# Kernel tuning notes

Hardware: AMD Instinct MI355X
Metric: run time of the kernel (lower is better)

Reference implementation:

```python
import jax, jax.numpy as jnp
import numpy as np

N_NODES = 100000
N_EDGES = 1600000
D_FEAT = 128
D_EMB = 128
ROUNDS = 4
M_OUT = 32
NUM_GRAPHS = 512


def setup_inputs() -> dict:
    key = jax.random.key(0)
    ks = jax.random.split(key, 12)
    x = jax.random.normal(ks[0], (N_NODES, D_FEAT), dtype=jnp.float32)
    edge_index = jax.random.randint(ks[1], (2, N_EDGES), 0, N_NODES, dtype=jnp.int32)
    batch = jnp.sort(jax.random.randint(ks[2], (N_NODES,), 0, NUM_GRAPHS, dtype=jnp.int32))
    s = 1.0 / np.sqrt(D_EMB)
    emb_W = jax.random.uniform(ks[3], (D_FEAT, D_EMB), minval=-s, maxval=s, dtype=jnp.float32)
    emb_b = jax.random.uniform(ks[4], (D_EMB,), minval=-s, maxval=s, dtype=jnp.float32)
    msg_W = jax.random.uniform(ks[5], (ROUNDS, D_EMB, D_EMB), minval=-s, maxval=s, dtype=jnp.float32)
    msg_b = jax.random.uniform(ks[6], (ROUNDS, D_EMB), minval=-s, maxval=s, dtype=jnp.float32)
    upd_W = jax.random.uniform(ks[7], (ROUNDS, D_EMB, D_EMB), minval=-s, maxval=s, dtype=jnp.float32)
    upd_b = jax.random.uniform(ks[8], (ROUNDS, D_EMB), minval=-s, maxval=s, dtype=jnp.float32)
    out_W = jax.random.uniform(ks[9], (D_EMB, M_OUT), minval=-s, maxval=s, dtype=jnp.float32)
    out_b = jax.random.uniform(ks[10], (M_OUT,), minval=-s, maxval=s, dtype=jnp.float32)
    return {"x": x, "edge_index": edge_index, "batch": batch,
            "emb_W": emb_W, "emb_b": emb_b, "msg_W": msg_W, "msg_b": msg_b,
            "upd_W": upd_W, "upd_b": upd_b, "out_W": out_W, "out_b": out_b}


def reference(x, edge_index, batch, emb_W, emb_b, msg_W, msg_b, upd_W, upd_b, out_W, out_b):
    src, dst = edge_index[0], edge_index[1]
    # initial node embedding: Linear + ReLU
    state = jax.nn.relu(x @ emb_W + emb_b)  # [N, D]
    for r in range(ROUNDS):
        message = jax.nn.relu(state @ msg_W[r] + msg_b[r])      # [N, D]
        # gather messages along edges, scatter-add to destination nodes
        aggregated = jax.ops.segment_sum(message[src], dst, num_segments=N_NODES)  # [N, D]
        state = state + jax.nn.relu(aggregated @ upd_W[r] + upd_b[r])
    # sum-pool nodes into graphs
    graph_state = jax.ops.segment_sum(state, batch, num_segments=NUM_GRAPHS)  # [G, D]
    return graph_state @ out_W + out_b  # [G, M]
```

## Files before the change

kernel.cpp:

```cpp
#include <hip/hip_runtime.h>

#define N_NODES    100000
#define N_EDGES    1600000
#define D_EMB      128
#define ROUNDS     4
#define M_OUT      32
#define NUM_GRAPHS 512

#define SCAN_ELEMS_PER_BLOCK 1024
#define SCAN_NBLK ((N_NODES + SCAN_ELEMS_PER_BLOCK - 1) / SCAN_ELEMS_PER_BLOCK)

typedef __attribute__((ext_vector_type(8))) short short8;
typedef __attribute__((ext_vector_type(4))) float f32x4;

static __device__ __forceinline__ unsigned short f2bf(float f) {
    union { float f; unsigned u; } v; v.f = f;
    unsigned u = v.u;
    unsigned r = (u + 0x7FFFu + ((u >> 16) & 1u)) >> 16;
    return (unsigned short)r;
}
static __device__ __forceinline__ float bf2f(unsigned short h) {
    union { unsigned u; float f; } v; v.u = ((unsigned)h) << 16;
    return v.f;
}

__global__ __launch_bounds__(256) void prep_weights_kernel(
    const float* __restrict__ emb_W, const float* __restrict__ msg_W,
    const float* __restrict__ upd_W, unsigned short* __restrict__ WTall)
{
    const int mi = blockIdx.x;
    const float* W = (mi == 0) ? emb_W
                   : (mi <= 4) ? msg_W + (size_t)(mi - 1) * D_EMB * D_EMB
                               : upd_W + (size_t)(mi - 5) * D_EMB * D_EMB;
    unsigned short* WT = WTall + (size_t)mi * D_EMB * D_EMB;
    for (int idx = threadIdx.x; idx < D_EMB * D_EMB; idx += 256) {
        const int n = idx >> 7, k = idx & 127;
        WT[idx] = f2bf(W[k * D_EMB + n]);
    }
}

template<int MODE, bool AF32>
__global__ __launch_bounds__(256) void gemm_mfma_kernel(
    const void* __restrict__ Aptr, const unsigned short* __restrict__ WT,
    const float* __restrict__ bias, float* __restrict__ state_f32,
    unsigned short* __restrict__ out_bf16)
{
    __shared__ unsigned short As[32][136];

    const int tid = threadIdx.x;
    const int r0  = blockIdx.x * 32;

    if (AF32) {
        const float4* A4 = (const float4*)Aptr + (size_t)r0 * 32;
        #pragma unroll
        for (int i = 0; i < 4; ++i) {
            const int ch = tid + (i << 8);
            const int r = ch >> 5, c = (ch & 31) << 2;
            const float4 f = A4[ch];
            ushort4 h;
            h.x = f2bf(f.x); h.y = f2bf(f.y); h.z = f2bf(f.z); h.w = f2bf(f.w);
            *(ushort4*)&As[r][c] = h;
        }
    } else {
        const uint4* A4 = (const uint4*)((const unsigned short*)Aptr + (size_t)r0 * D_EMB);
        #pragma unroll
        for (int i = 0; i < 2; ++i) {
            const int ch = tid + (i << 8);
            const int r = ch >> 4, c = (ch & 15) << 3;
            *(uint4*)&As[r][c] = A4[ch];
        }
    }
    __syncthreads();

    const int lane = tid & 63;
    const int w    = tid >> 6;
    const int m    = lane & 15;
    const int g    = lane >> 4;

    short8 a[2][4];
    #pragma unroll
    for (int rt = 0; rt < 2; ++rt)
        #pragma unroll
        for (int ks = 0; ks < 4; ++ks)
            a[rt][ks] = *(const short8*)&As[rt * 16 + m][ks * 32 + g * 8];

    short8 b[2][4];
    #pragma unroll
    for (int ct = 0; ct < 2; ++ct) {
        const int n = w * 32 + ct * 16 + m;
        #pragma unroll
        for (int ks = 0; ks < 4; ++ks)
            b[ct][ks] = *(const short8*)&WT[n * D_EMB + ks * 32 + g * 8];
    }

    f32x4 acc[2][2] = {};
    #pragma unroll
    for (int ks = 0; ks < 4; ++ks)
        #pragma unroll
        for (int rt = 0; rt < 2; ++rt)
            #pragma unroll
            for (int ct = 0; ct < 2; ++ct)
                acc[rt][ct] = __builtin_amdgcn_mfma_f32_16x16x32_bf16(
                    a[rt][ks], b[ct][ks], acc[rt][ct], 0, 0, 0);

    #pragma unroll
    for (int rt = 0; rt < 2; ++rt) {
        #pragma unroll
        for (int ct = 0; ct < 2; ++ct) {
            const int col = w * 32 + ct * 16 + m;
            const float bv = bias[col];
            #pragma unroll
            for (int r = 0; r < 4; ++r) {
                const int row = r0 + rt * 16 + g * 4 + r;
                const float v = fmaxf(acc[rt][ct][r] + bv, 0.f);
                const size_t idx = (size_t)row * D_EMB + col;
                if (MODE == 0) {
                    out_bf16[idx] = f2bf(v);
                } else if (MODE == 2) {
                    state_f32[idx] = v;
                    out_bf16[idx] = f2bf(v);
                } else {
                    const float s = state_f32[idx] + v;
                    state_f32[idx] = s;
                    out_bf16[idx] = f2bf(s);
                }
            }
        }
    }
}

__global__ __launch_bounds__(256) void hist_kernel(
    const int* __restrict__ dst, int* __restrict__ deg)
{
    const int e = blockIdx.x * 256 + threadIdx.x;
    if (e < N_EDGES) atomicAdd(&deg[dst[e]], 1);
}

__global__ __launch_bounds__(256) void scan_local_kernel(
    const int* __restrict__ deg, int* __restrict__ rp, int* __restrict__ partials)
{
    __shared__ int sm[256];
    const int tid  = threadIdx.x;
    const int base = blockIdx.x * SCAN_ELEMS_PER_BLOCK + tid * 4;

    int v0 = (base + 0 < N_NODES) ? deg[base + 0] : 0;
    int v1 = (base + 1 < N_NODES) ? deg[base + 1] : 0;
    int v2 = (base + 2 < N_NODES) ? deg[base + 2] : 0;
    int v3 = (base + 3 < N_NODES) ? deg[base + 3] : 0;
    const int tot = v0 + v1 + v2 + v3;

    sm[tid] = tot;
    __syncthreads();
    #pragma unroll
    for (int off = 1; off < 256; off <<= 1) {
        const int x = (tid >= off) ? sm[tid - off] : 0;
        __syncthreads();
        sm[tid] += x;
        __syncthreads();
    }
    const int bex = sm[tid] - tot;

    if (base + 0 < N_NODES) rp[base + 0] = bex;
    if (base + 1 < N_NODES) rp[base + 1] = bex + v0;
    if (base + 2 < N_NODES) rp[base + 2] = bex + v0 + v1;
    if (base + 3 < N_NODES) rp[base + 3] = bex + v0 + v1 + v2;
    if (tid == 255) partials[blockIdx.x] = sm[255];
}

__global__ __launch_bounds__(128) void scan_partials_kernel(int* __restrict__ partials)
{
    __shared__ int sm[128];
    const int tid = threadIdx.x;
    const int v = (tid < SCAN_NBLK) ? partials[tid] : 0;
    sm[tid] = v;
    __syncthreads();
    #pragma unroll
    for (int off = 1; off < 128; off <<= 1) {
        const int x = (tid >= off) ? sm[tid - off] : 0;
        __syncthreads();
        sm[tid] += x;
        __syncthreads();
    }
    if (tid < SCAN_NBLK) partials[tid] = sm[tid] - v;
}

__global__ __launch_bounds__(256) void scan_fixup_kernel(
    int* __restrict__ rp, const int* __restrict__ partials, int* __restrict__ pos)
{
    const int i = blockIdx.x * 256 + threadIdx.x;
    if (i < N_NODES) {
        const int v = rp[i] + partials[i >> 10];
        rp[i] = v;
        pos[i] = v;
    }
    if (i == 0) rp[N_NODES] = N_EDGES;
}

__global__ __launch_bounds__(256) void fill_kernel(
    const int* __restrict__ src, const int* __restrict__ dst,
    int* __restrict__ pos, int* __restrict__ esrc)
{
    const int e = blockIdx.x * 256 + threadIdx.x;
    if (e < N_EDGES) {
        const int idx = atomicAdd(&pos[dst[e]], 1);
        esrc[idx] = src[e];
    }
}

__global__ __launch_bounds__(256) void gather_bf16_kernel(
    const unsigned short* __restrict__ msg, const int* __restrict__ rp,
    const int* __restrict__ esrc, unsigned short* __restrict__ agg)
{
    const int tid = threadIdx.x;
    const int j   = tid & 15;
    const int n   = blockIdx.x * 16 + (tid >> 4);
    if (n >= N_NODES) return;

    const int beg = rp[n];
    const int end = rp[n + 1];
    const uint4* m4 = (const uint4*)msg;

    float a0[8] = {0,0,0,0,0,0,0,0};
    float a1[8] = {0,0,0,0,0,0,0,0};
    int i = beg;
    for (; i + 1 < end; i += 2) {
        const int s0 = esrc[i];
        const int s1 = esrc[i + 1];
        const uint4 v0 = m4[(size_t)s0 * 16 + j];
        const uint4 v1 = m4[(size_t)s1 * 16 + j];
        a0[0] += bf2f(v0.x & 0xffff); a0[1] += bf2f(v0.x >> 16);
        a0[2] += bf2f(v0.y & 0xffff); a0[3] += bf2f(v0.y >> 16);
        a0[4] += bf2f(v0.z & 0xffff); a0[5] += bf2f(v0.z >> 16);
        a0[6] += bf2f(v0.w & 0xffff); a0[7] += bf2f(v0.w >> 16);
        a1[0] += bf2f(v1.x & 0xffff); a1[1] += bf2f(v1.x >> 16);
        a1[2] += bf2f(v1.y & 0xffff); a1[3] += bf2f(v1.y >> 16);
        a1[4] += bf2f(v1.z & 0xffff); a1[5] += bf2f(v1.z >> 16);
        a1[6] += bf2f(v1.w & 0xffff); a1[7] += bf2f(v1.w >> 16);
    }
    if (i < end) {
        const uint4 v0 = m4[(size_t)esrc[i] * 16 + j];
        a0[0] += bf2f(v0.x & 0xffff); a0[1] += bf2f(v0.x >> 16);
        a0[2] += bf2f(v0.y & 0xffff); a0[3] += bf2f(v0.y >> 16);
        a0[4] += bf2f(v0.z & 0xffff); a0[5] += bf2f(v0.z >> 16);
        a0[6] += bf2f(v0.w & 0xffff); a0[7] += bf2f(v0.w >> 16);
    }
    #pragma unroll
    for (int t = 0; t < 8; ++t) a0[t] += a1[t];

    uint4 o;
    o.x = (unsigned)f2bf(a0[0]) | ((unsigned)f2bf(a0[1]) << 16);
    o.y = (unsigned)f2bf(a0[2]) | ((unsigned)f2bf(a0[3]) << 16);
    o.z = (unsigned)f2bf(a0[4]) | ((unsigned)f2bf(a0[5]) << 16);
    o.w = (unsigned)f2bf(a0[6]) | ((unsigned)f2bf(a0[7]) << 16);
    ((uint4*)agg)[(size_t)n * 16 + j] = o;
}

__global__ __launch_bounds__(256) void pool_kernel(
    const float* __restrict__ state, const int* __restrict__ batch,
    float* __restrict__ gs)
{
    const int tid = threadIdx.x;
    const int c = tid & 127;
    const int h = tid >> 7;
    const int n0 = blockIdx.x * 64 + h * 32;

    float acc = 0.f;
    int cur = -1;
    for (int i = 0; i < 32; ++i) {
        const int n = n0 + i;
        if (n >= N_NODES) break;
        const int bb = batch[n];
        if (bb != cur) {
            if (cur >= 0) unsafeAtomicAdd(&gs[cur * D_EMB + c], acc);
            cur = bb;
            acc = 0.f;
        }
        acc += state[(size_t)n * D_EMB + c];
    }
    if (cur >= 0) unsafeAtomicAdd(&gs[cur * D_EMB + c], acc);
}

__global__ __launch_bounds__(256) void out_kernel(
    const float* __restrict__ gs, const float* __restrict__ W,
    const float* __restrict__ bias, float* __restrict__ out)
{
    const int idx = blockIdx.x * 256 + threadIdx.x;
    const int g = idx >> 5;
    const int m = idx & 31;
    float acc = 0.f;
    #pragma unroll 8
    for (int k = 0; k < D_EMB; ++k)
        acc += gs[g * D_EMB + k] * W[k * M_OUT + m];
    out[idx] = acc + bias[m];
}

extern "C" void kernel_launch(void* const* d_in, const int* in_sizes, int n_in,
                              void* d_out, int out_size, void* d_ws, size_t ws_size,
                              hipStream_t stream)
{
    const float* x     = (const float*)d_in[0];
    const int*   eidx  = (const int*)d_in[1];
    const int*   batch = (const int*)d_in[2];
    const float* emb_W = (const float*)d_in[3];
    const float* emb_b = (const float*)d_in[4];
    const float* msg_W = (const float*)d_in[5];
    const float* msg_b = (const float*)d_in[6];
    const float* upd_W = (const float*)d_in[7];
    const float* upd_b = (const float*)d_in[8];
    const float* out_W = (const float*)d_in[9];
    const float* out_b = (const float*)d_in[10];
    float* out = (float*)d_out;

    const int* src = eidx;
    const int* dst = eidx + N_EDGES;

    char* p = (char*)d_ws;
    float* state_f32 = (float*)p;                       p += (size_t)N_NODES * D_EMB * 4;
    unsigned short* state_bf16 = (unsigned short*)p;    p += (size_t)N_NODES * D_EMB * 2;
    unsigned short* msg_bf16 = (unsigned short*)p;      p += (size_t)N_NODES * D_EMB * 2;
    unsigned short* agg_bf16 = (unsigned short*)p;      p += (size_t)N_NODES * D_EMB * 2;
    float* gs = (float*)p;                              p += (size_t)NUM_GRAPHS * D_EMB * 4;
    unsigned short* WTall = (unsigned short*)p;         p += (size_t)9 * D_EMB * D_EMB * 2;
    int* rp = (int*)p;                                  p += (size_t)(N_NODES + 1) * 4;
    int* esrc = (int*)p;                                p += (size_t)N_EDGES * 4;
    int* partials = (int*)p;

    int* deg = (int*)msg_bf16;
    int* pos = (int*)agg_bf16;

    const dim3 blk(256);
    const int gemm_grid = N_NODES / 32;

    prep_weights_kernel<<<9, blk, 0, stream>>>(emb_W, msg_W, upd_W, WTall);
    hipMemsetAsync(deg, 0, (size_t)N_NODES * sizeof(int), stream);
    hist_kernel<<<(N_EDGES + 255) / 256, blk, 0, stream>>>(dst, deg);
    scan_local_kernel<<<SCAN_NBLK, blk, 0, stream>>>(deg, rp, partials);
    scan_partials_kernel<<<1, 128, 0, stream>>>(partials);
    scan_fixup_kernel<<<(SCAN_NBLK * SCAN_ELEMS_PER_BLOCK) / 256, blk, 0, stream>>>(rp, partials, pos);
    fill_kernel<<<(N_EDGES + 255) / 256, blk, 0, stream>>>(src, dst, pos, esrc);

    gemm_mfma_kernel<2, true><<<gemm_grid, blk, 0, stream>>>(
        x, WTall, emb_b, state_f32, state_bf16);

    for (int r = 0; r < ROUNDS; ++r) {
        gemm_mfma_kernel<0, false><<<gemm_grid, blk, 0, stream>>>(
            state_bf16, WTall + (size_t)(1 + r) * D_EMB * D_EMB,
            msg_b + (size_t)r * D_EMB, nullptr, msg_bf16);
        gather_bf16_kernel<<<(N_NODES + 15) / 16, blk, 0, stream>>>(
            msg_bf16, rp, esrc, agg_bf16);
        gemm_mfma_kernel<1, false><<<gemm_grid, blk, 0, stream>>>(
            agg_bf16, WTall + (size_t)(5 + r) * D_EMB * D_EMB,
            upd_b + (size_t)r * D_EMB, state_f32, state_bf16);
    }

    hipMemsetAsync(gs, 0, (size_t)NUM_GRAPHS * D_EMB * sizeof(float), stream);
    pool_kernel<<<(N_NODES + 63) / 64, blk, 0, stream>>>(state_f32, batch, gs);
    out_kernel<<<(NUM_GRAPHS * M_OUT) / 256, blk, 0, stream>>>(gs, out_W, out_b, out);
}
```

Measured before the change: 700.8 us.

## Use persistent double-buffered GEMM, bf16-only state, and multipass CSR build

The GEMM becomes a persistent kernel of 1024 blocks. Each block loads its weight fragments once and double-buffers the A tiles through shared memory, prefetching the next tile into registers. The fp32 state copy is dropped and the residual state is kept only in bf16, which cuts write and read traffic in the update GEMM and in pooling, at the cost of extra rounding across rounds. The histogram and CSR fill kernels now make 8 passes, each restricted to one destination range, to localise atomics. The pool kernel reads the bf16 state two channels per thread.

```diff
diff --git a/kernel.cpp b/kernel.cpp
--- a/kernel.cpp
+++ b/kernel.cpp
@@ -6,6 +6,11 @@
 #define ROUNDS     4
 #define M_OUT      32
 #define NUM_GRAPHS 512
+
+#define NPASS      8
+#define PASS_RANGE (N_NODES / NPASS)
+#define GEMM_BLOCKS 1024
+#define N_TILES    (N_NODES / 32)
 
 #define SCAN_ELEMS_PER_BLOCK 1024
 #define SCAN_NBLK ((N_NODES + SCAN_ELEMS_PER_BLOCK - 1) / SCAN_ELEMS_PER_BLOCK)
@@ -40,100 +45,148 @@
 }
 
 template<int MODE, bool AF32>
-__global__ __launch_bounds__(256) void gemm_mfma_kernel(
+__global__ __launch_bounds__(256) void gemm_loop_kernel(
     const void* __restrict__ Aptr, const unsigned short* __restrict__ WT,
-    const float* __restrict__ bias, float* __restrict__ state_f32,
-    unsigned short* __restrict__ out_bf16)
-{
-    __shared__ unsigned short As[32][136];
-
-    const int tid = threadIdx.x;
-    const int r0  = blockIdx.x * 32;
-
-    if (AF32) {
-        const float4* A4 = (const float4*)Aptr + (size_t)r0 * 32;
-        #pragma unroll
-        for (int i = 0; i < 4; ++i) {
-            const int ch = tid + (i << 8);
-            const int r = ch >> 5, c = (ch & 31) << 2;
-            const float4 f = A4[ch];
-            ushort4 h;
-            h.x = f2bf(f.x); h.y = f2bf(f.y); h.z = f2bf(f.z); h.w = f2bf(f.w);
-            *(ushort4*)&As[r][c] = h;
-        }
-    } else {
-        const uint4* A4 = (const uint4*)((const unsigned short*)Aptr + (size_t)r0 * D_EMB);
-        #pragma unroll
-        for (int i = 0; i < 2; ++i) {
-            const int ch = tid + (i << 8);
-            const int r = ch >> 4, c = (ch & 15) << 3;
-            *(uint4*)&As[r][c] = A4[ch];
-        }
-    }
-    __syncthreads();
-
+    const float* __restrict__ bias, unsigned short* __restrict__ state,
+    unsigned short* __restrict__ outb)
+{
+    __shared__ unsigned short As[2][32][136];
+
+    const int tid  = threadIdx.x;
     const int lane = tid & 63;
     const int w    = tid >> 6;
     const int m    = lane & 15;
     const int g    = lane >> 4;
 
-    short8 a[2][4];
-    #pragma unroll
-    for (int rt = 0; rt < 2; ++rt)
-        #pragma unroll
-        for (int ks = 0; ks < 4; ++ks)
-            a[rt][ks] = *(const short8*)&As[rt * 16 + m][ks * 32 + g * 8];
-
-    short8 b[2][4];
+    short8 bfr[2][4];
     #pragma unroll
     for (int ct = 0; ct < 2; ++ct) {
         const int n = w * 32 + ct * 16 + m;
         #pragma unroll
         for (int ks = 0; ks < 4; ++ks)
-            b[ct][ks] = *(const short8*)&WT[n * D_EMB + ks * 32 + g * 8];
-    }
-
-    f32x4 acc[2][2] = {};
-    #pragma unroll
-    for (int ks = 0; ks < 4; ++ks)
+            bfr[ct][ks] = *(const short8*)&WT[n * D_EMB + ks * 32 + g * 8];
+    }
+    const float bv0 = bias[w * 32 + m];
+    const float bv1 = bias[w * 32 + 16 + m];
+
+    int tile = blockIdx.x;
+
+    if (AF32) {
+        const float4* A4 = (const float4*)Aptr;
+        #pragma unroll
+        for (int i = 0; i < 4; ++i) {
+            const int ch = tid + (i << 8);
+            const float4 f = A4[(size_t)tile * 1024 + ch];
+            ushort4 h; h.x = f2bf(f.x); h.y = f2bf(f.y); h.z = f2bf(f.z); h.w = f2bf(f.w);
+            *(ushort4*)&As[0][ch >> 5][(ch & 31) << 2] = h;
+        }
+    } else {
+        const uint4* A2 = (const uint4*)Aptr;
+        #pragma unroll
+        for (int i = 0; i < 2; ++i) {
+            const int ch = tid + (i << 8);
+            const uint4 v = A2[(size_t)tile * 512 + ch];
+            *(uint4*)&As[0][ch >> 4][(ch & 15) << 3] = v;
+        }
+    }
+    __syncthreads();
+
+    int cur = 0;
+    while (true) {
+        const int next = tile + GEMM_BLOCKS;
+        const bool have = next < N_TILES;
+
+        float4 rgf[4]; uint4 rgu[2];
+        if (have) {
+            if (AF32) {
+                const float4* A4 = (const float4*)Aptr;
+                #pragma unroll
+                for (int i = 0; i < 4; ++i)
+                    rgf[i] = A4[(size_t)next * 1024 + tid + (i << 8)];
+            } else {
+                const uint4* A2 = (const uint4*)Aptr;
+                #pragma unroll
+                for (int i = 0; i < 2; ++i)
+                    rgu[i] = A2[(size_t)next * 512 + tid + (i << 8)];
+            }
+        }
+
+        short8 a[2][4];
         #pragma unroll
         for (int rt = 0; rt < 2; ++rt)
             #pragma unroll
-            for (int ct = 0; ct < 2; ++ct)
-                acc[rt][ct] = __builtin_amdgcn_mfma_f32_16x16x32_bf16(
-                    a[rt][ks], b[ct][ks], acc[rt][ct], 0, 0, 0);
-
-    #pragma unroll
-    for (int rt = 0; rt < 2; ++rt) {
-        #pragma unroll
-        for (int ct = 0; ct < 2; ++ct) {
-            const int col = w * 32 + ct * 16 + m;
-            const float bv = bias[col];
+            for (int ks = 0; ks < 4; ++ks)
+                a[rt][ks] = *(const short8*)&As[cur][rt * 16 + m][ks * 32 + g * 8];
+
+        f32x4 acc[2][2] = {};
+        #pragma unroll
+        for (int ks = 0; ks < 4; ++ks)
             #pragma unroll
-            for (int r = 0; r < 4; ++r) {
-                const int row = r0 + rt * 16 + g * 4 + r;
-                const float v = fmaxf(acc[rt][ct][r] + bv, 0.f);
-                const size_t idx = (size_t)row * D_EMB + col;
-                if (MODE == 0) {
-                    out_bf16[idx] = f2bf(v);
-                } else if (MODE == 2) {
-                    state_f32[idx] = v;
-                    out_bf16[idx] = f2bf(v);
-                } else {
-                    const float s = state_f32[idx] + v;
-                    state_f32[idx] = s;
-                    out_bf16[idx] = f2bf(s);
+            for (int rt = 0; rt < 2; ++rt)
+                #pragma unroll
+                for (int ct = 0; ct < 2; ++ct)
+                    acc[rt][ct] = __builtin_amdgcn_mfma_f32_16x16x32_bf16(
+                        a[rt][ks], bfr[ct][ks], acc[rt][ct], 0, 0, 0);
+
+        if (have) {
+            if (AF32) {
+                #pragma unroll
+                for (int i = 0; i < 4; ++i) {
+                    const int ch = tid + (i << 8);
+                    ushort4 h;
+                    h.x = f2bf(rgf[i].x); h.y = f2bf(rgf[i].y);
+                    h.z = f2bf(rgf[i].z); h.w = f2bf(rgf[i].w);
+                    *(ushort4*)&As[cur ^ 1][ch >> 5][(ch & 31) << 2] = h;
+                }
+            } else {
+                #pragma unroll
+                for (int i = 0; i < 2; ++i) {
+                    const int ch = tid + (i << 8);
+                    *(uint4*)&As[cur ^ 1][ch >> 4][(ch & 15) << 3] = rgu[i];
                 }
             }
         }
-    }
-}
-
-__global__ __launch_bounds__(256) void hist_kernel(
+
+        #pragma unroll
+        for (int rt = 0; rt < 2; ++rt) {
+            #pragma unroll
+            for (int ct = 0; ct < 2; ++ct) {
+                const int col = w * 32 + ct * 16 + m;
+                const float bv = ct ? bv1 : bv0;
+                #pragma unroll
+                for (int r = 0; r < 4; ++r) {
+                    const int row = tile * 32 + rt * 16 + g * 4 + r;
+                    const size_t idx = (size_t)row * D_EMB + col;
+                    const float v = fmaxf(acc[rt][ct][r] + bv, 0.f);
+                    if (MODE == 0) {
+                        outb[idx] = f2bf(v);
+                    } else if (MODE == 2) {
+                        state[idx] = f2bf(v);
+                    } else {
+                        const float s = bf2f(state[idx]) + v;
+                        state[idx] = f2bf(s);
+                    }
+                }
+            }
+        }
+
+        if (!have) break;
+        __syncthreads();
+        cur ^= 1;
+        tile = next;
+    }
+}
+
+__global__ __launch_bounds__(256) void hist_mp_kernel(
     const int* __restrict__ dst, int* __restrict__ deg)
 {
-    const int e = blockIdx.x * 256 + threadIdx.x;
-    if (e < N_EDGES) atomicAdd(&deg[dst[e]], 1);
+    const int p = blockIdx.x & 7;
+    const int e = (blockIdx.x >> 3) * 256 + threadIdx.x;
+    if (e < N_EDGES) {
+        const int d = dst[e];
+        if ((unsigned)(d - p * PASS_RANGE) < (unsigned)PASS_RANGE)
+            atomicAdd(&deg[d], 1);
+    }
 }
 
 __global__ __launch_bounds__(256) void scan_local_kernel(
@@ -196,14 +249,18 @@
     if (i == 0) rp[N_NODES] = N_EDGES;
 }
 
-__global__ __launch_bounds__(256) void fill_kernel(
+__global__ __launch_bounds__(256) void fill_mp_kernel(
     const int* __restrict__ src, const int* __restrict__ dst,
     int* __restrict__ pos, int* __restrict__ esrc)
 {
-    const int e = blockIdx.x * 256 + threadIdx.x;
+    const int p = blockIdx.x & 7;
+    const int e = (blockIdx.x >> 3) * 256 + threadIdx.x;
     if (e < N_EDGES) {
-        const int idx = atomicAdd(&pos[dst[e]], 1);
-        esrc[idx] = src[e];
+        const int d = dst[e];
+        if ((unsigned)(d - p * PASS_RANGE) < (unsigned)PASS_RANGE) {
+            const int idx = atomicAdd(&pos[d], 1);
+            esrc[idx] = src[e];
+        }
     }
 }
 
@@ -256,28 +313,35 @@
 }
 
 __global__ __launch_bounds__(256) void pool_kernel(
-    const float* __restrict__ state, const int* __restrict__ batch,
+    const unsigned short* __restrict__ state, const int* __restrict__ batch,
     float* __restrict__ gs)
 {
-    const int tid = threadIdx.x;
-    const int c = tid & 127;
-    const int h = tid >> 7;
-    const int n0 = blockIdx.x * 64 + h * 32;
-
-    float acc = 0.f;
+    const int lane = threadIdx.x & 63;
+    const int grp  = threadIdx.x >> 6;
+    const int n0 = blockIdx.x * 128 + grp * 32;
+    const int c0 = lane * 2;
+
+    float a0 = 0.f, a1 = 0.f;
     int cur = -1;
     for (int i = 0; i < 32; ++i) {
         const int n = n0 + i;
         if (n >= N_NODES) break;
         const int bb = batch[n];
         if (bb != cur) {
-            if (cur >= 0) unsafeAtomicAdd(&gs[cur * D_EMB + c], acc);
-            cur = bb;
-            acc = 0.f;
-        }
-        acc += state[(size_t)n * D_EMB + c];
-    }
-    if (cur >= 0) unsafeAtomicAdd(&gs[cur * D_EMB + c], acc);
+            if (cur >= 0) {
+                unsafeAtomicAdd(&gs[cur * D_EMB + c0],     a0);
+                unsafeAtomicAdd(&gs[cur * D_EMB + c0 + 1], a1);
+            }
+            cur = bb; a0 = 0.f; a1 = 0.f;
+        }
+        const unsigned u = *(const unsigned*)&state[(size_t)n * D_EMB + c0];
+        a0 += bf2f(u & 0xffff);
+        a1 += bf2f(u >> 16);
+    }
+    if (cur >= 0) {
+        unsafeAtomicAdd(&gs[cur * D_EMB + c0],     a0);
+        unsafeAtomicAdd(&gs[cur * D_EMB + c0 + 1], a1);
+    }
 }
 
 __global__ __launch_bounds__(256) void out_kernel(
@@ -315,45 +379,44 @@
     const int* dst = eidx + N_EDGES;
 
     char* p = (char*)d_ws;
-    float* state_f32 = (float*)p;                       p += (size_t)N_NODES * D_EMB * 4;
-    unsigned short* state_bf16 = (unsigned short*)p;    p += (size_t)N_NODES * D_EMB * 2;
-    unsigned short* msg_bf16 = (unsigned short*)p;      p += (size_t)N_NODES * D_EMB * 2;
-    unsigned short* agg_bf16 = (unsigned short*)p;      p += (size_t)N_NODES * D_EMB * 2;
-    float* gs = (float*)p;                              p += (size_t)NUM_GRAPHS * D_EMB * 4;
-    unsigned short* WTall = (unsigned short*)p;         p += (size_t)9 * D_EMB * D_EMB * 2;
-    int* rp = (int*)p;                                  p += (size_t)(N_NODES + 1) * 4;
-    int* esrc = (int*)p;                                p += (size_t)N_EDGES * 4;
+    unsigned short* state = (unsigned short*)p;   p += (size_t)N_NODES * D_EMB * 2;
+    unsigned short* msg   = (unsigned short*)p;   p += (size_t)N_NODES * D_EMB * 2;
+    unsigned short* agg   = (unsigned short*)p;   p += (size_t)N_NODES * D_EMB * 2;
+    float* gs = (float*)p;                        p += (size_t)NUM_GRAPHS * D_EMB * 4;
+    unsigned short* WTall = (unsigned short*)p;   p += (size_t)9 * D_EMB * D_EMB * 2;
+    int* rp       = (int*)p;                      p += (size_t)(N_NODES + 1) * 4;
+    int* esrc     = (int*)p;                      p += (size_t)N_EDGES * 4;
     int* partials = (int*)p;
 
-    int* deg = (int*)msg_bf16;
-    int* pos = (int*)agg_bf16;
+    int* deg = (int*)msg;
+    int* pos = (int*)agg;
 
     const dim3 blk(256);
-    const int gemm_grid = N_NODES / 32;
+    const int mp_grid = (N_EDGES / 256) * NPASS;
 
     prep_weights_kernel<<<9, blk, 0, stream>>>(emb_W, msg_W, upd_W, WTall);
     hipMemsetAsync(deg, 0, (size_t)N_NODES * sizeof(int), stream);
-    hist_kernel<<<(N_EDGES + 255) / 256, blk, 0, stream>>>(dst, deg);
+    hist_mp_kernel<<<mp_grid, blk, 0, stream>>>(dst, deg);
     scan_local_kernel<<<SCAN_NBLK, blk, 0, stream>>>(deg, rp, partials);
     scan_partials_kernel<<<1, 128, 0, stream>>>(partials);
     scan_fixup_kernel<<<(SCAN_NBLK * SCAN_ELEMS_PER_BLOCK) / 256, blk, 0, stream>>>(rp, partials, pos);
-    fill_kernel<<<(N_EDGES + 255) / 256, blk, 0, stream>>>(src, dst, pos, esrc);
-
-    gemm_mfma_kernel<2, true><<<gemm_grid, blk, 0, stream>>>(
-        x, WTall, emb_b, state_f32, state_bf16);
+    fill_mp_kernel<<<mp_grid, blk, 0, stream>>>(src, dst, pos, esrc);
+
+    gemm_loop_kernel<2, true><<<GEMM_BLOCKS, blk, 0, stream>>>(
+        x, WTall, emb_b, state, nullptr);
 
     for (int r = 0; r < ROUNDS; ++r) {
-        gemm_mfma_kernel<0, false><<<gemm_grid, blk, 0, stream>>>(
-            state_bf16, WTall + (size_t)(1 + r) * D_EMB * D_EMB,
-            msg_b + (size_t)r * D_EMB, nullptr, msg_bf16);
+        gemm_loop_kernel<0, false><<<GEMM_BLOCKS, blk, 0, stream>>>(
+            state, WTall + (size_t)(1 + r) * D_EMB * D_EMB,
+            msg_b + (size_t)r * D_EMB, nullptr, msg);
         gather_bf16_kernel<<<(N_NODES + 15) / 16, blk, 0, stream>>>(
-            msg_bf16, rp, esrc, agg_bf16);
-        gemm_mfma_kernel<1, false><<<gemm_grid, blk, 0, stream>>>(
-            agg_bf16, WTall + (size_t)(5 + r) * D_EMB * D_EMB,
-            upd_b + (size_t)r * D_EMB, state_f32, state_bf16);
+            msg, rp, esrc, agg);
+        gemm_loop_kernel<1, false><<<GEMM_BLOCKS, blk, 0, stream>>>(
+            agg, WTall + (size_t)(5 + r) * D_EMB * D_EMB,
+            upd_b + (size_t)r * D_EMB, state, nullptr);
     }
 
     hipMemsetAsync(gs, 0, (size_t)NUM_GRAPHS * D_EMB * sizeof(float), stream);
-    pool_kernel<<<(N_NODES + 63) / 64, blk, 0, stream>>>(state_f32, batch, gs);
+    pool_kernel<<<(N_NODES + 127) / 128, blk, 0, stream>>>(state, batch, gs);
     out_kernel<<<(NUM_GRAPHS * M_OUT) / 256, blk, 0, stream>>>(gs, out_W, out_b, out);
 }
```

Measured after the change: 572.3 us. -18.3%, faster.
